# Performance work log

Hardware: AMD Instinct MI355X
Metric: run time of the kernel (lower is better)

Reference implementation:

```python
import jax, jax.numpy as jnp
import numpy as np
import math

N_USER = 100000
N_GAME = 50000
E = 200000
D = 256          # in_dim == out_dim
H = 8            # num_heads
SCALE = math.sqrt(D // H)  # sqrt(head_dim) = sqrt(32)


def setup_inputs() -> dict:
    key = jax.random.key(0)
    keys = jax.random.split(key, 64)
    it = iter(range(64))
    def nk():
        return keys[next(it)]
    s = 1.0 / math.sqrt(D)
    inp = {}
    inp["x_user"] = jax.random.normal(nk(), (N_USER, D), dtype=jnp.float32)
    inp["x_game"] = jax.random.normal(nk(), (N_GAME, D), dtype=jnp.float32)
    # node-type projections (k/q/v/out) for user and game
    for nt in ("user", "game"):
        for p in ("k", "q", "v", "out"):
            inp[f"W{p}_{nt}"] = jax.random.normal(nk(), (D, D), dtype=jnp.float32) * s
            inp[f"b{p}_{nt}"] = jax.random.normal(nk(), (D,), dtype=jnp.float32) * 0.01
    # edge-type attention + message transforms
    for et in ("played", "rev"):
        inp[f"Wa_{et}"] = jax.random.normal(nk(), (D, H), dtype=jnp.float32) * s
        inp[f"ba_{et}"] = jax.random.normal(nk(), (H,), dtype=jnp.float32) * 0.01
        inp[f"Wm_{et}"] = jax.random.normal(nk(), (D, D), dtype=jnp.float32) * s
        inp[f"bm_{et}"] = jax.random.normal(nk(), (D,), dtype=jnp.float32) * 0.01
    # edge indices: played (user -> game), rev_played (game -> user)
    inp["ei_played_src"] = jax.random.randint(nk(), (E,), 0, N_USER, dtype=jnp.int32)
    inp["ei_played_dst"] = jax.random.randint(nk(), (E,), 0, N_GAME, dtype=jnp.int32)
    inp["ei_rev_src"] = jax.random.randint(nk(), (E,), 0, N_GAME, dtype=jnp.int32)
    inp["ei_rev_dst"] = jax.random.randint(nk(), (E,), 0, N_USER, dtype=jnp.int32)
    return inp


def _lin(x, W, b):
    return x @ W + b


def _edge_pass(k_src_all, q_dst_all, v_src_all, Wa, ba, Wm, bm, src, dst, n_dst):
    # gather per-edge K/Q/V                                   [E, D]
    k_src = k_src_all[src]
    q_dst = q_dst_all[dst]
    v_src = v_src_all[src]
    # attention score MLP over head dim                       [E, H]
    scores = ((k_src * q_dst) @ Wa + ba) / SCALE
    attn = jax.nn.softmax(scores, axis=-1)  # softmax over heads (as in source)
    # message MLP                                             [E, D]
    msgs = v_src @ Wm + bm
    weighted = msgs * attn.mean(axis=-1, keepdims=True)
    # scatter-add to destination nodes
    agg = jax.ops.segment_sum(weighted, dst, num_segments=n_dst)
    cnt = jax.ops.segment_sum(jnp.ones((dst.shape[0], 1), weighted.dtype), dst, num_segments=n_dst)
    return agg, cnt


def reference(x_user, x_game,
              Wk_user, bk_user, Wq_user, bq_user, Wv_user, bv_user, Wout_user, bout_user,
              Wk_game, bk_game, Wq_game, bq_game, Wv_game, bv_game, Wout_game, bout_game,
              Wa_played, ba_played, Wm_played, bm_played,
              Wa_rev, ba_rev, Wm_rev, bm_rev,
              ei_played_src, ei_played_dst, ei_rev_src, ei_rev_dst):
    # per-node-type K/Q/V projections
    k_u = _lin(x_user, Wk_user, bk_user)
    q_u = _lin(x_user, Wq_user, bq_user)
    v_u = _lin(x_user, Wv_user, bv_user)
    k_g = _lin(x_game, Wk_game, bk_game)
    q_g = _lin(x_game, Wq_game, bq_game)
    v_g = _lin(x_game, Wv_game, bv_game)

    # user --played--> game
    agg_game, cnt_game = _edge_pass(k_u, q_g, v_u, Wa_played, ba_played, Wm_played, bm_played,
                                    ei_played_src, ei_played_dst, N_GAME)
    # game --rev_played--> user
    agg_user, cnt_user = _edge_pass(k_g, q_u, v_g, Wa_rev, ba_rev, Wm_rev, bm_rev,
                                    ei_rev_src, ei_rev_dst, N_USER)

    def finish(agg, cnt, x, Wout, bout):
        normed = agg / jnp.maximum(cnt, 1.0)
        return jax.nn.relu(_lin(normed, Wout, bout) + x)

    out_user = finish(agg_user, cnt_user, x_user, Wout_user, bout_user)
    out_game = finish(agg_game, cnt_game, x_game, Wout_game, bout_game)
    # concatenate node types for a single output array [N_USER+N_GAME, D]
    return jnp.concatenate([out_user, out_game], axis=0)
```

## Files before the change

kernel.cpp:

```cpp
#include <hip/hip_runtime.h>
#include <cstddef>
#include <cstdint>


#define DD 256
#define SCAN_CHUNK 2048
#define NCONV 2048

typedef __attribute__((ext_vector_type(8))) short short8;
typedef __attribute__((ext_vector_type(4))) float floatx4;
typedef __attribute__((ext_vector_type(4))) short shortx4;

__device__ __forceinline__ short f2bf(float f) {
    union { float f; unsigned u; } c;
    c.f = f;
    unsigned r = c.u + 0x7fffu + ((c.u >> 16) & 1u);
    return (short)(r >> 16);
}
__device__ __forceinline__ float bflo(unsigned u) {
    union { unsigned u; float f; } c;
    c.u = u << 16;
    return c.f;
}
__device__ __forceinline__ float bfhi(unsigned u) {
    union { unsigned u; float f; } c;
    c.u = u & 0xffff0000u;
    return c.f;
}

__global__ __launch_bounds__(256) void fuseA(const float* __restrict__ A0,
                                             const float* __restrict__ B0,
                                             float* __restrict__ C0,
                                             const float* __restrict__ A1,
                                             const float* __restrict__ B1,
                                             float* __restrict__ C1,
                                             const int* __restrict__ dst0,
                                             int* __restrict__ cnt0, int E0,
                                             const int* __restrict__ dst1,
                                             int* __restrict__ cnt1, int E1) {
    __shared__ float As[DD];
    const int bid = blockIdx.x;
    const int c = threadIdx.x;
    if (bid < 512) {
        const int which = bid >> 8;
        const int r = bid & 255;
        const float* A = which ? A1 : A0;
        const float* B = which ? B1 : B0;
        float* C = which ? C1 : C0;
        As[c] = A[r * DD + c];
        __syncthreads();
        float acc = 0.f;
#pragma unroll 8
        for (int k = 0; k < DD; ++k) acc += As[k] * B[k * DD + c];
        C[r * DD + c] = acc;
    } else {
        const int nb0 = (E0 + 255) >> 8;
        const int b = bid - 512;
        if (b < nb0) {
            const int i = b * 256 + c;
            if (i < E0) atomicAdd(&cnt0[dst0[i]], 1);
        } else {
            const int i = (b - nb0) * 256 + c;
            if (i < E1) atomicAdd(&cnt1[dst1[i]], 1);
        }
    }
}

__global__ __launch_bounds__(256) void fuseB(const float* __restrict__ A0,
                                             const float* __restrict__ B0,
                                             short* __restrict__ C0,
                                             const float* __restrict__ A1,
                                             const float* __restrict__ B1,
                                             short* __restrict__ C1,
                                             int* __restrict__ off_g,
                                             int* __restrict__ sums_g, int n_g,
                                             int* __restrict__ off_u,
                                             int* __restrict__ sums_u, int n_u) {
    __shared__ float As[DD];
    __shared__ int ls[256];
    const int bid = blockIdx.x;
    const int tid = threadIdx.x;
    if (bid < 512) {
        const int which = bid >> 8;
        const int r = bid & 255;
        const int c = tid;
        const float* A = which ? A1 : A0;
        const float* B = which ? B1 : B0;
        short* C = which ? C1 : C0;
        As[c] = A[r * DD + c];
        __syncthreads();
        float acc = 0.f;
#pragma unroll 8
        for (int k = 0; k < DD; ++k) acc += As[k] * B[k * DD + c];
        const int idx = ((((r >> 5) * 16 + (c >> 4)) * 64 +
                          ((c & 15) | (((r >> 3) & 3) << 4))) << 3) + (r & 7);
        C[idx] = f2bf(acc * 0.125f);
    } else {
        const int nch_g = (n_g + SCAN_CHUNK - 1) / SCAN_CHUNK;
        const int b = bid - 512;
        int* off;
        int* sums;
        int n, cb;
        if (b < nch_g) { off = off_g; sums = sums_g; n = n_g; cb = b; }
        else { off = off_u; sums = sums_u; n = n_u; cb = b - nch_g; }
        const int base = cb * SCAN_CHUNK + tid * 8;
        int v[8];
        int s = 0;
#pragma unroll
        for (int i = 0; i < 8; ++i) {
            const int idx = base + i;
            v[i] = (idx < n) ? off[idx] : 0;
            s += v[i];
        }
        ls[tid] = s;
        __syncthreads();
        for (int d = 1; d < 256; d <<= 1) {
            const int t = (tid >= d) ? ls[tid - d] : 0;
            __syncthreads();
            ls[tid] += t;
            __syncthreads();
        }
        int excl = tid ? ls[tid - 1] : 0;
        if (tid == 255) sums[cb] = ls[255];
#pragma unroll
        for (int i = 0; i < 8; ++i) {
            const int idx = base + i;
            if (idx < n) off[idx] = excl;
            excl += v[i];
        }
    }
}

__global__ __launch_bounds__(256) void fuseC(const float* __restrict__ bv0,
                                             const float* __restrict__ Wm0,
                                             const float* __restrict__ bm0,
                                             const float* __restrict__ Wout0,
                                             float* __restrict__ bb0,
                                             const float* __restrict__ bv1,
                                             const float* __restrict__ Wm1,
                                             const float* __restrict__ bm1,
                                             const float* __restrict__ Wout1,
                                             float* __restrict__ bb1,
                                             int* __restrict__ sums_g, int nch_g,
                                             int* __restrict__ sums_u, int nch_u) {
    __shared__ float t[DD];
    __shared__ int ls[256];
    const int tid = threadIdx.x;
    if (blockIdx.x < 2) {
        const int w = blockIdx.x;
        const float* bv = w ? bv1 : bv0;
        const float* Wm = w ? Wm1 : Wm0;
        const float* bm = w ? bm1 : bm0;
        const float* Wout = w ? Wout1 : Wout0;
        float* bb = w ? bb1 : bb0;
        float acc = bm[tid];
#pragma unroll 8
        for (int k = 0; k < DD; ++k) acc += bv[k] * Wm[k * DD + tid];
        t[tid] = acc;
        __syncthreads();
        float acc2 = 0.f;
#pragma unroll 8
        for (int k = 0; k < DD; ++k) acc2 += t[k] * Wout[k * DD + tid];
        bb[tid] = acc2 * 0.125f;
    } else {
        int* sums = (blockIdx.x == 2) ? sums_g : sums_u;
        const int nch = (blockIdx.x == 2) ? nch_g : nch_u;
        ls[tid] = (tid < nch) ? sums[tid] : 0;
        __syncthreads();
        for (int d = 1; d < 256; d <<= 1) {
            const int t2 = (tid >= d) ? ls[tid - d] : 0;
            __syncthreads();
            ls[tid] += t2;
            __syncthreads();
        }
        if (tid < nch) sums[tid] = tid ? ls[tid - 1] : 0;
    }
}

__global__ __launch_bounds__(256) void fuseD(int* __restrict__ off_g,
                                             const int* __restrict__ sums_g,
                                             int* __restrict__ cur_g, int n_g, int Eg,
                                             int* __restrict__ off_u,
                                             const int* __restrict__ sums_u,
                                             int* __restrict__ cur_u, int n_u, int Eu) {
    const int gidx = blockIdx.x * 256 + threadIdx.x;
    const int span_g = n_g + 1;
    if (gidx < span_g) {
        if (gidx < n_g) {
            const int v = off_g[gidx] + sums_g[gidx / SCAN_CHUNK];
            off_g[gidx] = v;
            cur_g[gidx] = v;
        } else {
            off_g[n_g] = Eg;
        }
    } else {
        const int idx = gidx - span_g;
        if (idx < n_u) {
            const int v = off_u[idx] + sums_u[idx / SCAN_CHUNK];
            off_u[idx] = v;
            cur_u[idx] = v;
        } else if (idx == n_u) {
            off_u[n_u] = Eu;
        }
    }
}

__global__ __launch_bounds__(256) void fuseE(const int* __restrict__ src0,
                                             const int* __restrict__ dst0,
                                             int* __restrict__ cur0,
                                             int* __restrict__ perm0, int E0,
                                             const int* __restrict__ src1,
                                             const int* __restrict__ dst1,
                                             int* __restrict__ cur1,
                                             int* __restrict__ perm1, int E1,
                                             const float* __restrict__ xu,
                                             const float* __restrict__ xg,
                                             short* __restrict__ xbf,
                                             int n_user, int n_game) {
    const int nb0 = (E0 + 255) >> 8;
    const int nb1 = (E1 + 255) >> 8;
    const int nbperm = nb0 + nb1;
    const int b = blockIdx.x;
    const int tid = threadIdx.x;
    if (b < nb0) {
        const int i = b * 256 + tid;
        if (i < E0) {
            const int pos = atomicAdd(&cur0[dst0[i]], 1);
            perm0[pos] = src0[i];
        }
    } else if (b < nbperm) {
        const int i = (b - nb0) * 256 + tid;
        if (i < E1) {
            const int pos = atomicAdd(&cur1[dst1[i]], 1);
            perm1[pos] = src1[i];
        }
    } else {
        const size_t u4 = (size_t)n_user * 64;
        const size_t tot4 = u4 + (size_t)n_game * 64;
        const size_t stride = (size_t)NCONV * 256;
        for (size_t i = (size_t)(b - nbperm) * 256 + tid; i < tot4; i += stride) {
            floatx4 v;
            if (i < u4)
                v = __builtin_nontemporal_load((const floatx4*)xu + i);
            else
                v = __builtin_nontemporal_load((const floatx4*)xg + (i - u4));
            shortx4 b4;
            b4.x = f2bf(v.x);
            b4.y = f2bf(v.y);
            b4.z = f2bf(v.z);
            b4.w = f2bf(v.w);
            *((shortx4*)xbf + i) = b4;
        }
    }
}

__global__ __launch_bounds__(256, 4) void agg_gemm6(
    const short* __restrict__ xbf,
    const float* __restrict__ x_user, const float* __restrict__ x_game,
    const int* __restrict__ perm_rev, const int* __restrict__ off_user,
    const short* __restrict__ Bsw_rev, const float* __restrict__ bb_rev,
    const float* __restrict__ bout_user,
    const int* __restrict__ perm_played, const int* __restrict__ off_game,
    const short* __restrict__ Bsw_played, const float* __restrict__ bb_played,
    const float* __restrict__ bout_game,
    float* __restrict__ outp, int n_user, int n_game, int nb_game) {
    __shared__ short As[32][264];
    __shared__ float bt[32];

    const int tid = threadIdx.x;
    const int wave = __builtin_amdgcn_readfirstlane(tid >> 6);
    const int lane = tid & 63;

    const short* xb_src;
    const float* x_res;
    const int* perm;
    const int* off;
    const short* Bsw;
    const float* bb;
    const float* bout;
    float* out;
    int M, r0;
    if ((int)blockIdx.x < nb_game) {
        xb_src = xbf;
        x_res = x_game;
        perm = perm_played; off = off_game;
        Bsw = Bsw_played; bb = bb_played; bout = bout_game;
        out = outp + (size_t)n_user * DD;
        M = n_game;
        r0 = (int)blockIdx.x * 32;
    } else {
        xb_src = xbf + (size_t)n_user * DD;
        x_res = x_user;
        perm = perm_rev; off = off_user;
        Bsw = Bsw_rev; bb = bb_rev; bout = bout_user;
        out = outp;
        M = n_user;
        r0 = ((int)blockIdx.x - nb_game) * 32;
    }

    int eb[8], deg[8];
    int s0[8], s1[8];
    float4 acc[8];
#pragma unroll
    for (int j = 0; j < 8; ++j) {
        const int r = r0 + wave * 8 + j;
        eb[j] = (r < M) ? off[r] : 0;
        const int e1 = (r < M) ? off[r + 1] : 0;
        deg[j] = e1 - eb[j];
        acc[j].x = 0.f; acc[j].y = 0.f; acc[j].z = 0.f; acc[j].w = 0.f;
        if (lane == 0) bt[wave * 8 + j] = (deg[j] > 0) ? 1.0f : 0.0f;
    }
#pragma unroll
    for (int j = 0; j < 8; ++j) {
        s0[j] = (deg[j] > 0) ? perm[eb[j]] : 0;
        s1[j] = (deg[j] > 1) ? perm[eb[j] + 1] : 0;
    }
    int mdeg = 0;
#pragma unroll
    for (int j = 0; j < 8; ++j) mdeg = max(mdeg, deg[j]);

    for (int t = 0; t < mdeg; ++t) {
        uint2 d[8];
        bool h[8];
#pragma unroll
        for (int j = 0; j < 8; ++j) {
            h[j] = t < deg[j];
            if (h[j])
                d[j] = *((const uint2*)(xb_src + (size_t)s0[j] * DD) + lane);
        }
        int s2[8];
#pragma unroll
        for (int j = 0; j < 8; ++j)
            s2[j] = (t + 2 < deg[j]) ? perm[eb[j] + t + 2] : 0;
#pragma unroll
        for (int j = 0; j < 8; ++j) {
            if (h[j]) {
                acc[j].x += bflo(d[j].x);
                acc[j].y += bfhi(d[j].x);
                acc[j].z += bflo(d[j].y);
                acc[j].w += bfhi(d[j].y);
            }
            s0[j] = s1[j];
            s1[j] = s2[j];
        }
    }
#pragma unroll
    for (int j = 0; j < 8; ++j) {
        const int lr = wave * 8 + j;
        const float inv = 1.0f / fmaxf((float)deg[j], 1.0f);
        short4 b4;
        b4.x = f2bf(acc[j].x * inv);
        b4.y = f2bf(acc[j].y * inv);
        b4.z = f2bf(acc[j].z * inv);
        b4.w = f2bf(acc[j].w * inv);
        *(short4*)&As[lr][lane * 4] = b4;
    }
    __syncthreads();

    const int quad = lane >> 4;
    const int l16 = lane & 15;
    floatx4 cacc[2][4];
#pragma unroll
    for (int rt = 0; rt < 2; ++rt)
#pragma unroll
        for (int ct = 0; ct < 4; ++ct) cacc[rt][ct] = (floatx4){0.f, 0.f, 0.f, 0.f};

    for (int kb8 = 0; kb8 < 8; ++kb8) {
        short8 af[2];
#pragma unroll
        for (int rt = 0; rt < 2; ++rt)
            af[rt] = *(const short8*)&As[rt * 16 + l16][kb8 * 32 + quad * 8];
        short8 bf[4];
        const short* bp = Bsw + (((size_t)(kb8 * 16 + wave * 4) * 64 + lane) << 3);
#pragma unroll
        for (int ct = 0; ct < 4; ++ct)
            bf[ct] = *(const short8*)(bp + (ct << 9));
#pragma unroll
        for (int rt = 0; rt < 2; ++rt)
#pragma unroll
            for (int ct = 0; ct < 4; ++ct)
                cacc[rt][ct] = __builtin_amdgcn_mfma_f32_16x16x32_bf16(
                    af[rt], bf[ct], cacc[rt][ct], 0, 0, 0);
    }

    float bbv[4], bov[4];
#pragma unroll
    for (int ct = 0; ct < 4; ++ct) {
        const int n = wave * 64 + ct * 16 + l16;
        bbv[ct] = bb[n];
        bov[ct] = bout[n];
    }
#pragma unroll
    for (int rt = 0; rt < 2; ++rt) {
#pragma unroll
        for (int j = 0; j < 4; ++j) {
            const int lr = rt * 16 + quad * 4 + j;
            const int r = r0 + lr;
            if (r < M) {
                const float btv = bt[lr];
                const float* xr = x_res + (size_t)r * DD;
                float* orow = out + (size_t)r * DD;
#pragma unroll
                for (int ct = 0; ct < 4; ++ct) {
                    const int n = wave * 64 + ct * 16 + l16;
                    const float xv = __builtin_nontemporal_load(xr + n);
                    const float o = cacc[rt][ct][j] + btv * bbv[ct] + bov[ct] + xv;
                    __builtin_nontemporal_store(fmaxf(o, 0.f), orow + n);
                }
            }
        }
    }
}

extern "C" void kernel_launch(void* const* d_in, const int* in_sizes, int n_in,
                              void* d_out, int out_size, void* d_ws, size_t ws_size,
                              hipStream_t stream) {
    const float* x_user = (const float*)d_in[0];
    const float* x_game = (const float*)d_in[1];
    const float* Wv_user = (const float*)d_in[6];
    const float* bv_user = (const float*)d_in[7];
    const float* Wout_user = (const float*)d_in[8];
    const float* bout_user = (const float*)d_in[9];
    const float* Wv_game = (const float*)d_in[14];
    const float* bv_game = (const float*)d_in[15];
    const float* Wout_game = (const float*)d_in[16];
    const float* bout_game = (const float*)d_in[17];
    const float* Wm_played = (const float*)d_in[20];
    const float* bm_played = (const float*)d_in[21];
    const float* Wm_rev = (const float*)d_in[24];
    const float* bm_rev = (const float*)d_in[25];
    const int* ei_played_src = (const int*)d_in[26];
    const int* ei_played_dst = (const int*)d_in[27];
    const int* ei_rev_src = (const int*)d_in[28];
    const int* ei_rev_dst = (const int*)d_in[29];

    const int n_user = in_sizes[0] / DD;
    const int n_game = in_sizes[1] / DD;
    const int e_played = in_sizes[26];
    const int e_rev = in_sizes[28];

    float* out = (float*)d_out;

    float* fws = (float*)d_ws;
    float* T0 = fws;
    float* T1 = T0 + DD * DD;
    float* bb_played = T1 + DD * DD;
    float* bb_rev = bb_played + DD;
    short* Bsw_played = (short*)(bb_rev + DD);
    short* Bsw_rev = Bsw_played + DD * DD;
    int* iws = (int*)(Bsw_rev + DD * DD);
    int* off_game = iws;
    int* off_user = off_game + (n_game + 1);
    int* cursor_game = off_user + (n_user + 1);
    int* cursor_user = cursor_game + n_game;
    int* sums_game = cursor_user + n_user;
    int* sums_user = sums_game + 256;
    int* perm_played = sums_user + 256;
    int* perm_rev = perm_played + e_played;
    uintptr_t xaddr = (uintptr_t)(perm_rev + e_rev);
    xaddr = (xaddr + 255) & ~(uintptr_t)255;
    short* xbf = (short*)xaddr;
    (void)ws_size; (void)n_in; (void)out_size;

    hipMemsetAsync(off_game, 0, (size_t)(n_game + n_user + 2) * sizeof(int), stream);

    const int nbh_p = (e_played + 255) / 256;
    const int nbh_r = (e_rev + 255) / 256;
    const int nch_g = (n_game + SCAN_CHUNK - 1) / SCAN_CHUNK;
    const int nch_u = (n_user + SCAN_CHUNK - 1) / SCAN_CHUNK;

    fuseA<<<512 + nbh_p + nbh_r, 256, 0, stream>>>(
        Wv_user, Wm_played, T0, Wv_game, Wm_rev, T1,
        ei_played_dst, off_game, e_played, ei_rev_dst, off_user, e_rev);
    fuseB<<<512 + nch_g + nch_u, 256, 0, stream>>>(
        T0, Wout_game, Bsw_played, T1, Wout_user, Bsw_rev,
        off_game, sums_game, n_game, off_user, sums_user, n_user);
    fuseC<<<4, 256, 0, stream>>>(
        bv_user, Wm_played, bm_played, Wout_game, bb_played,
        bv_game, Wm_rev, bm_rev, Wout_user, bb_rev,
        sums_game, nch_g, sums_user, nch_u);
    const int ntot = (n_game + 1) + (n_user + 1);
    fuseD<<<(ntot + 255) / 256, 256, 0, stream>>>(
        off_game, sums_game, cursor_game, n_game, e_played,
        off_user, sums_user, cursor_user, n_user, e_rev);
    fuseE<<<nbh_p + nbh_r + NCONV, 256, 0, stream>>>(
        ei_played_src, ei_played_dst, cursor_game, perm_played, e_played,
        ei_rev_src, ei_rev_dst, cursor_user, perm_rev, e_rev,
        x_user, x_game, xbf, n_user, n_game);

    const int nb_game = (n_game + 31) / 32;
    const int nb_user = (n_user + 31) / 32;
    agg_gemm6<<<nb_game + nb_user, 256, 0, stream>>>(
        xbf, x_user, x_game, perm_rev, off_user, Bsw_rev, bb_rev, bout_user,
        perm_played, off_game, Bsw_played, bb_played, bout_game,
        out, n_user, n_game, nb_game);
}
```

Baseline: 498.7 us.

## Merge bias and bf16 conversion into first kernel, fold scan, deepen gather prefetch

The fuseC kernel is removed. Its bias-vector computation now runs inside fuseA, and its chunk-sum scan is redone redundantly in shared memory by every fuseD block. The fp32-to-bf16 conversion of the node features moves from fuseE to fuseA, so it overlaps with the weight products and degree counting. The aggregation loop now double-buffers the gathered rows so the next neighbor's data loads while the current one is accumulated. Together these save one launch and give more memory-level parallelism in the gather, at the cost of more registers and a larger first kernel.

```diff
diff --git a/kernel.cpp b/kernel.cpp
--- a/kernel.cpp
+++ b/kernel.cpp
@@ -28,19 +28,24 @@
     return c.f;
 }
 
-__global__ __launch_bounds__(256) void fuseA(const float* __restrict__ A0,
-                                             const float* __restrict__ B0,
-                                             float* __restrict__ C0,
-                                             const float* __restrict__ A1,
-                                             const float* __restrict__ B1,
-                                             float* __restrict__ C1,
-                                             const int* __restrict__ dst0,
-                                             int* __restrict__ cnt0, int E0,
-                                             const int* __restrict__ dst1,
-                                             int* __restrict__ cnt1, int E1) {
+__global__ __launch_bounds__(256) void fuseA(
+    const float* __restrict__ A0, const float* __restrict__ B0, float* __restrict__ C0,
+    const float* __restrict__ A1, const float* __restrict__ B1, float* __restrict__ C1,
+    const float* __restrict__ bv0, const float* __restrict__ Wm0,
+    const float* __restrict__ bm0, const float* __restrict__ Wout0,
+    float* __restrict__ bb0,
+    const float* __restrict__ bv1, const float* __restrict__ Wm1,
+    const float* __restrict__ bm1, const float* __restrict__ Wout1,
+    float* __restrict__ bb1,
+    const int* __restrict__ dst0, int* __restrict__ cnt0, int E0,
+    const int* __restrict__ dst1, int* __restrict__ cnt1, int E1,
+    const float* __restrict__ xu, const float* __restrict__ xg,
+    short* __restrict__ xbf, int n_user, int n_game) {
     __shared__ float As[DD];
     const int bid = blockIdx.x;
     const int c = threadIdx.x;
+    const int nb0 = (E0 + 255) >> 8;
+    const int nb1 = (E1 + 255) >> 8;
     if (bid < 512) {
         const int which = bid >> 8;
         const int r = bid & 255;
@@ -53,15 +58,48 @@
 #pragma unroll 8
         for (int k = 0; k < DD; ++k) acc += As[k] * B[k * DD + c];
         C[r * DD + c] = acc;
-    } else {
-        const int nb0 = (E0 + 255) >> 8;
-        const int b = bid - 512;
+    } else if (bid < 514) {
+        const int w = bid - 512;
+        const float* bv = w ? bv1 : bv0;
+        const float* Wm = w ? Wm1 : Wm0;
+        const float* bm = w ? bm1 : bm0;
+        const float* Wout = w ? Wout1 : Wout0;
+        float* bb = w ? bb1 : bb0;
+        float acc = bm[c];
+#pragma unroll 8
+        for (int k = 0; k < DD; ++k) acc += bv[k] * Wm[k * DD + c];
+        As[c] = acc;
+        __syncthreads();
+        float acc2 = 0.f;
+#pragma unroll 8
+        for (int k = 0; k < DD; ++k) acc2 += As[k] * Wout[k * DD + c];
+        bb[c] = acc2 * 0.125f;
+    } else if (bid < 514 + nb0 + nb1) {
+        const int b = bid - 514;
         if (b < nb0) {
             const int i = b * 256 + c;
             if (i < E0) atomicAdd(&cnt0[dst0[i]], 1);
         } else {
             const int i = (b - nb0) * 256 + c;
             if (i < E1) atomicAdd(&cnt1[dst1[i]], 1);
+        }
+    } else {
+        const size_t u4 = (size_t)n_user * 64;
+        const size_t tot4 = u4 + (size_t)n_game * 64;
+        const size_t stride = (size_t)NCONV * 256;
+        for (size_t i = (size_t)(bid - 514 - nb0 - nb1) * 256 + c; i < tot4;
+             i += stride) {
+            floatx4 v;
+            if (i < u4)
+                v = __builtin_nontemporal_load((const floatx4*)xu + i);
+            else
+                v = __builtin_nontemporal_load((const floatx4*)xg + (i - u4));
+            shortx4 b4;
+            b4.x = f2bf(v.x);
+            b4.y = f2bf(v.y);
+            b4.z = f2bf(v.z);
+            b4.w = f2bf(v.w);
+            *((shortx4*)xbf + i) = b4;
         }
     }
 }
@@ -131,63 +169,38 @@
     }
 }
 
-__global__ __launch_bounds__(256) void fuseC(const float* __restrict__ bv0,
-                                             const float* __restrict__ Wm0,
-                                             const float* __restrict__ bm0,
-                                             const float* __restrict__ Wout0,
-                                             float* __restrict__ bb0,
-                                             const float* __restrict__ bv1,
-                                             const float* __restrict__ Wm1,
-                                             const float* __restrict__ bm1,
-                                             const float* __restrict__ Wout1,
-                                             float* __restrict__ bb1,
-                                             int* __restrict__ sums_g, int nch_g,
-                                             int* __restrict__ sums_u, int nch_u) {
-    __shared__ float t[DD];
-    __shared__ int ls[256];
-    const int tid = threadIdx.x;
-    if (blockIdx.x < 2) {
-        const int w = blockIdx.x;
-        const float* bv = w ? bv1 : bv0;
-        const float* Wm = w ? Wm1 : Wm0;
-        const float* bm = w ? bm1 : bm0;
-        const float* Wout = w ? Wout1 : Wout0;
-        float* bb = w ? bb1 : bb0;
-        float acc = bm[tid];
-#pragma unroll 8
-        for (int k = 0; k < DD; ++k) acc += bv[k] * Wm[k * DD + tid];
-        t[tid] = acc;
-        __syncthreads();
-        float acc2 = 0.f;
-#pragma unroll 8
-        for (int k = 0; k < DD; ++k) acc2 += t[k] * Wout[k * DD + tid];
-        bb[tid] = acc2 * 0.125f;
-    } else {
-        int* sums = (blockIdx.x == 2) ? sums_g : sums_u;
-        const int nch = (blockIdx.x == 2) ? nch_g : nch_u;
-        ls[tid] = (tid < nch) ? sums[tid] : 0;
-        __syncthreads();
-        for (int d = 1; d < 256; d <<= 1) {
-            const int t2 = (tid >= d) ? ls[tid - d] : 0;
-            __syncthreads();
-            ls[tid] += t2;
-            __syncthreads();
-        }
-        if (tid < nch) sums[tid] = tid ? ls[tid - 1] : 0;
-    }
-}
-
 __global__ __launch_bounds__(256) void fuseD(int* __restrict__ off_g,
                                              const int* __restrict__ sums_g,
                                              int* __restrict__ cur_g, int n_g, int Eg,
                                              int* __restrict__ off_u,
                                              const int* __restrict__ sums_u,
-                                             int* __restrict__ cur_u, int n_u, int Eu) {
-    const int gidx = blockIdx.x * 256 + threadIdx.x;
+                                             int* __restrict__ cur_u, int n_u, int Eu,
+                                             int nch_g, int nch_u) {
+    __shared__ int ls[128];
+    const int tid = threadIdx.x;
+    if (tid < 128) {
+        int v = 0;
+        if (tid < 64) {
+            if (tid < nch_g) v = sums_g[tid];
+        } else {
+            if (tid - 64 < nch_u) v = sums_u[tid - 64];
+        }
+        ls[tid] = v;
+    }
+    __syncthreads();
+    for (int d = 1; d < 64; d <<= 1) {
+        int t2 = 0;
+        if (tid < 128 && (tid & 63) >= d) t2 = ls[tid - d];
+        __syncthreads();
+        if (tid < 128) ls[tid] += t2;
+        __syncthreads();
+    }
+    const int gidx = blockIdx.x * 256 + tid;
     const int span_g = n_g + 1;
     if (gidx < span_g) {
         if (gidx < n_g) {
-            const int v = off_g[gidx] + sums_g[gidx / SCAN_CHUNK];
+            const int cg = gidx / SCAN_CHUNK;
+            const int v = off_g[gidx] + (cg ? ls[cg - 1] : 0);
             off_g[gidx] = v;
             cur_g[gidx] = v;
         } else {
@@ -196,7 +209,8 @@
     } else {
         const int idx = gidx - span_g;
         if (idx < n_u) {
-            const int v = off_u[idx] + sums_u[idx / SCAN_CHUNK];
+            const int cu = idx / SCAN_CHUNK;
+            const int v = off_u[idx] + (cu ? ls[64 + cu - 1] : 0);
             off_u[idx] = v;
             cur_u[idx] = v;
         } else if (idx == n_u) {
@@ -212,14 +226,8 @@
                                              const int* __restrict__ src1,
                                              const int* __restrict__ dst1,
                                              int* __restrict__ cur1,
-                                             int* __restrict__ perm1, int E1,
-                                             const float* __restrict__ xu,
-                                             const float* __restrict__ xg,
-                                             short* __restrict__ xbf,
-                                             int n_user, int n_game) {
+                                             int* __restrict__ perm1, int E1) {
     const int nb0 = (E0 + 255) >> 8;
-    const int nb1 = (E1 + 255) >> 8;
-    const int nbperm = nb0 + nb1;
     const int b = blockIdx.x;
     const int tid = threadIdx.x;
     if (b < nb0) {
@@ -228,33 +236,16 @@
             const int pos = atomicAdd(&cur0[dst0[i]], 1);
             perm0[pos] = src0[i];
         }
-    } else if (b < nbperm) {
+    } else {
         const int i = (b - nb0) * 256 + tid;
         if (i < E1) {
             const int pos = atomicAdd(&cur1[dst1[i]], 1);
             perm1[pos] = src1[i];
         }
-    } else {
-        const size_t u4 = (size_t)n_user * 64;
-        const size_t tot4 = u4 + (size_t)n_game * 64;
-        const size_t stride = (size_t)NCONV * 256;
-        for (size_t i = (size_t)(b - nbperm) * 256 + tid; i < tot4; i += stride) {
-            floatx4 v;
-            if (i < u4)
-                v = __builtin_nontemporal_load((const floatx4*)xu + i);
-            else
-                v = __builtin_nontemporal_load((const floatx4*)xg + (i - u4));
-            shortx4 b4;
-            b4.x = f2bf(v.x);
-            b4.y = f2bf(v.y);
-            b4.z = f2bf(v.z);
-            b4.w = f2bf(v.w);
-            *((shortx4*)xbf + i) = b4;
-        }
-    }
-}
-
-__global__ __launch_bounds__(256, 4) void agg_gemm6(
+    }
+}
+
+__global__ __launch_bounds__(256, 4) void agg_gemm7(
     const short* __restrict__ xbf,
     const float* __restrict__ x_user, const float* __restrict__ x_game,
     const int* __restrict__ perm_rev, const int* __restrict__ off_user,
@@ -299,7 +290,8 @@
     }
 
     int eb[8], deg[8];
-    int s0[8], s1[8];
+    int sB[8];
+    uint2 dA[8], dB[8];
     float4 acc[8];
 #pragma unroll
     for (int j = 0; j < 8; ++j) {
@@ -312,36 +304,53 @@
     }
 #pragma unroll
     for (int j = 0; j < 8; ++j) {
-        s0[j] = (deg[j] > 0) ? perm[eb[j]] : 0;
-        s1[j] = (deg[j] > 1) ? perm[eb[j] + 1] : 0;
-    }
+        if (deg[j] > 0) {
+            const int sA = perm[eb[j]];
+            dA[j] = *((const uint2*)(xb_src + (size_t)sA * DD) + lane);
+        }
+    }
+#pragma unroll
+    for (int j = 0; j < 8; ++j) sB[j] = (deg[j] > 1) ? perm[eb[j] + 1] : 0;
+
     int mdeg = 0;
 #pragma unroll
     for (int j = 0; j < 8; ++j) mdeg = max(mdeg, deg[j]);
 
-    for (int t = 0; t < mdeg; ++t) {
-        uint2 d[8];
-        bool h[8];
+    for (int t = 0; t < mdeg; t += 2) {
+#pragma unroll
+        for (int j = 0; j < 8; ++j)
+            if (t + 1 < deg[j])
+                dB[j] = *((const uint2*)(xb_src + (size_t)sB[j] * DD) + lane);
+        int sC[8];
+#pragma unroll
+        for (int j = 0; j < 8; ++j)
+            sC[j] = (t + 2 < deg[j]) ? perm[eb[j] + t + 2] : 0;
 #pragma unroll
         for (int j = 0; j < 8; ++j) {
-            h[j] = t < deg[j];
-            if (h[j])
-                d[j] = *((const uint2*)(xb_src + (size_t)s0[j] * DD) + lane);
-        }
-        int s2[8];
+            if (t < deg[j]) {
+                acc[j].x += bflo(dA[j].x);
+                acc[j].y += bfhi(dA[j].x);
+                acc[j].z += bflo(dA[j].y);
+                acc[j].w += bfhi(dA[j].y);
+            }
+        }
 #pragma unroll
         for (int j = 0; j < 8; ++j)
-            s2[j] = (t + 2 < deg[j]) ? perm[eb[j] + t + 2] : 0;
+            if (t + 2 < deg[j])
+                dA[j] = *((const uint2*)(xb_src + (size_t)sC[j] * DD) + lane);
+        int sD[8];
+#pragma unroll
+        for (int j = 0; j < 8; ++j)
+            sD[j] = (t + 3 < deg[j]) ? perm[eb[j] + t + 3] : 0;
 #pragma unroll
         for (int j = 0; j < 8; ++j) {
-            if (h[j]) {
-                acc[j].x += bflo(d[j].x);
-                acc[j].y += bfhi(d[j].x);
-                acc[j].z += bflo(d[j].y);
-                acc[j].w += bfhi(d[j].y);
+            if (t + 1 < deg[j]) {
+                acc[j].x += bflo(dB[j].x);
+                acc[j].y += bfhi(dB[j].x);
+                acc[j].z += bflo(dB[j].y);
+                acc[j].w += bfhi(dB[j].y);
             }
-            s0[j] = s1[j];
-            s1[j] = s2[j];
+            sB[j] = sD[j];
         }
     }
 #pragma unroll
@@ -469,28 +478,26 @@
     const int nch_g = (n_game + SCAN_CHUNK - 1) / SCAN_CHUNK;
     const int nch_u = (n_user + SCAN_CHUNK - 1) / SCAN_CHUNK;
 
-    fuseA<<<512 + nbh_p + nbh_r, 256, 0, stream>>>(
+    fuseA<<<512 + 2 + nbh_p + nbh_r + NCONV, 256, 0, stream>>>(
         Wv_user, Wm_played, T0, Wv_game, Wm_rev, T1,
-        ei_played_dst, off_game, e_played, ei_rev_dst, off_user, e_rev);
+        bv_user, Wm_played, bm_played, Wout_game, bb_played,
+        bv_game, Wm_rev, bm_rev, Wout_user, bb_rev,
+        ei_played_dst, off_game, e_played, ei_rev_dst, off_user, e_rev,
+        x_user, x_game, xbf, n_user, n_game);
     fuseB<<<512 + nch_g + nch_u, 256, 0, stream>>>(
         T0, Wout_game, Bsw_played, T1, Wout_user, Bsw_rev,
         off_game, sums_game, n_game, off_user, sums_user, n_user);
-    fuseC<<<4, 256, 0, stream>>>(
-        bv_user, Wm_played, bm_played, Wout_game, bb_played,
-        bv_game, Wm_rev, bm_rev, Wout_user, bb_rev,
-        sums_game, nch_g, sums_user, nch_u);
     const int ntot = (n_game + 1) + (n_user + 1);
     fuseD<<<(ntot + 255) / 256, 256, 0, stream>>>(
         off_game, sums_game, cursor_game, n_game, e_played,
-        off_user, sums_user, cursor_user, n_user, e_rev);
-    fuseE<<<nbh_p + nbh_r + NCONV, 256, 0, stream>>>(
+        off_user, sums_user, cursor_user, n_user, e_rev, nch_g, nch_u);
+    fuseE<<<nbh_p + nbh_r, 256, 0, stream>>>(
         ei_played_src, ei_played_dst, cursor_game, perm_played, e_played,
-        ei_rev_src, ei_rev_dst, cursor_user, perm_rev, e_rev,
-        x_user, x_game, xbf, n_user, n_game);
+        ei_rev_src, ei_rev_dst, cursor_user, perm_rev, e_rev);
 
     const int nb_game = (n_game + 31) / 32;
     const int nb_user = (n_user + 31) / 32;
-    agg_gemm6<<<nb_game + nb_user, 256, 0, stream>>>(
+    agg_gemm7<<<nb_game + nb_user, 256, 0, stream>>>(
         xbf, x_user, x_game, perm_rev, off_user, Bsw_rev, bb_rev, bout_user,
         perm_played, off_game, Bsw_played, bb_played, bout_game,
         out, n_user, n_game, nb_game);
```

Measured after the change: 480.8 us. -3.6%, faster.
